# Kernel tuning notes

Hardware: AMD Instinct MI355X
Metric: run time of the kernel (lower is better)

Reference implementation:

```python
import jax, jax.numpy as jnp
import numpy as np

B, S, H, NH, DH, I, C, P = 4, 1024, 1280, 20, 64, 5120, 13, 8
LN_EPS = 1e-5


def setup_inputs() -> dict:
    key = jax.random.key(0)
    ks = jax.random.split(key, 20)
    n = lambda k, shp, s=0.02: (jax.random.normal(k, shp, jnp.float32) * s)
    return {
        "hidden_states": jax.random.normal(ks[0], (B, S, H), jnp.float32),
        "attention_mask": jnp.ones((B, S), jnp.float32),
        "Wq": n(ks[1], (H, H)), "bq": jnp.zeros((H,), jnp.float32),
        "Wk": n(ks[2], (H, H)), "bk": jnp.zeros((H,), jnp.float32),
        "Wv": n(ks[3], (H, H)), "bv": jnp.zeros((H,), jnp.float32),
        "W_ct1": n(ks[4], (P, C), 0.3), "b_ct1": jnp.zeros((P,), jnp.float32),
        "W_ct2": n(ks[5], (P, C), 0.3), "b_ct2": jnp.zeros((P,), jnp.float32),
        "M": n(ks[6], (C, C), 0.5),
        "bias_scale": jnp.full((1,), 0.5, jnp.float32),
        "W_ptm": n(ks[7], (P, H)), "b_ptm": jnp.zeros((P,), jnp.float32),
        "ln_g": jnp.ones((H,), jnp.float32), "ln_b": jnp.zeros((H,), jnp.float32),
        "Wf1": n(ks[8], (I, H)), "bf1": jnp.zeros((I,), jnp.float32),
        "Wf2": n(ks[9], (H, I)), "bf2": jnp.zeros((H,), jnp.float32),
    }


def reference(hidden_states, attention_mask, Wq, bq, Wk, bk, Wv, bv,
              W_ct1, b_ct1, W_ct2, b_ct2, M, bias_scale, W_ptm, b_ptm,
              ln_g, ln_b, Wf1, bf1, Wf2, bf2):
    h = hidden_states
    # crosstalk bilinear projection: (P,C) @ (C,P) -> (P,P)
    out1 = (M.T @ W_ct1.T + b_ct1).T          # (P, C)
    out2 = M @ W_ct2.T + b_ct2                # (C, P)
    R = out1 @ out2                           # (P, P)
    # ptm_predictor (Linear H->P) + softmax
    ptm = jax.nn.softmax(h @ W_ptm.T + b_ptm, axis=-1)            # (B,S,P)
    Bb = jnp.tanh(jnp.einsum('blc,cd,bmd->blm', ptm, R, ptm)) * bias_scale  # (B,S,S)
    # manual multi-head attention
    q = (h @ Wq.T + bq).reshape(B, S, NH, DH).transpose(0, 2, 1, 3)
    k = (h @ Wk.T + bk).reshape(B, S, NH, DH).transpose(0, 2, 1, 3)
    v = (h @ Wv.T + bv).reshape(B, S, NH, DH).transpose(0, 2, 1, 3)
    scores = jnp.einsum('bhld,bhmd->bhlm', q, k) / np.float32(np.sqrt(DH))
    scores = scores + Bb[:, None]
    scores = scores + (1.0 - attention_mask)[:, None, None, :] * jnp.finfo(h.dtype).min
    probs = jax.nn.softmax(scores, axis=-1)
    ctx = jnp.einsum('bhlm,bhmd->bhld', probs, v)
    ctx = ctx.transpose(0, 2, 1, 3).reshape(B, S, H)
    # residual + LayerNorm
    x = h + ctx
    mu = jnp.mean(x, -1, keepdims=True)
    var = jnp.var(x, -1, keepdims=True)
    x = (x - mu) * jax.lax.rsqrt(var + LN_EPS) * ln_g + ln_b
    # FFN with exact GELU, residual
    ff = jax.nn.gelu(x @ Wf1.T + bf1, approximate=False) @ Wf2.T + bf2
    return x + ff
```

## Files before the change

kernel.cpp:

```cpp
#include <hip/hip_runtime.h>
#include <math.h>

typedef _Float16 f16;
typedef _Float16 f16x2 __attribute__((ext_vector_type(2)));
typedef _Float16 f16x8 __attribute__((ext_vector_type(8)));
typedef _Float16 f16x4 __attribute__((ext_vector_type(4)));
typedef float f32x4 __attribute__((ext_vector_type(4)));

#define B_ 4
#define S_ 1024
#define H_ 1280
#define NH_ 20
#define DH_ 64
#define I_ 5120
#define C_ 13
#define P_ 8
#define QS_ 3840
#define LOG2E 1.44269504088896f

__device__ __forceinline__ void store_val(float* p, float v) { *p = v; }
__device__ __forceinline__ void store_val(f16* p, float v) { *p = (f16)v; }

__device__ __forceinline__ float fast_gelu(float x) {
    float ax = 0.70710678118654752f * fabsf(x);
    float t = __builtin_amdgcn_rcpf(1.0f + 0.3275911f * ax);
    float p = t * (0.254829592f + t * (-0.284496736f + t * (1.421413741f
              + t * (-1.453152027f + t * 1.061405429f))));
    float e = __builtin_exp2f(-(LOG2E) * ax * ax);
    float er = 1.0f - p * e;
    float cdf = 0.5f + 0.5f * (x >= 0.0f ? er : -er);
    return x * cdf;
}

__device__ __forceinline__ float fast_tanh(float x) {
    x = fminf(fmaxf(x, -20.0f), 20.0f);
    float e = __builtin_exp2f(x * (2.0f * LOG2E));
    return (e - 1.0f) * __builtin_amdgcn_rcpf(e + 1.0f);
}

__global__ __launch_bounds__(256) void cvt5_kernel(
    const float* __restrict__ s0, f16* __restrict__ d0, int n0,
    const float* __restrict__ s1, f16* __restrict__ d1, int n1,
    const float* __restrict__ s2, f16* __restrict__ d2, int n2,
    const float* __restrict__ s3, f16* __restrict__ d3, int n3,
    const float* __restrict__ s4, f16* __restrict__ d4, int n4) {
    int seg = blockIdx.y;
    const float* src = (seg == 0) ? s0 : (seg == 1) ? s1 : (seg == 2) ? s2
                     : (seg == 3) ? s3 : s4;
    f16* dst = (seg == 0) ? d0 : (seg == 1) ? d1 : (seg == 2) ? d2
             : (seg == 3) ? d3 : d4;
    int n = (seg == 0) ? n0 : (seg == 1) ? n1 : (seg == 2) ? n2
          : (seg == 3) ? n3 : n4;
    int i = blockIdx.x * 256 + threadIdx.x;
    if (i < n) {
        f32x4 v = ((const f32x4*)src)[i];
        f16x4 o;
#pragma unroll
        for (int e = 0; e < 4; e++) o[e] = (f16)v[e];
        ((f16x4*)dst)[i] = o;
    }
}

__global__ __launch_bounds__(256) void ptm_kernel(const float* __restrict__ hin,
                                                  const float* __restrict__ Wptm,
                                                  const float* __restrict__ bptm,
                                                  const float* __restrict__ Mg,
                                                  const float* __restrict__ W1,
                                                  const float* __restrict__ b1,
                                                  const float* __restrict__ W2,
                                                  const float* __restrict__ b2,
                                                  float* __restrict__ ptm,
                                                  float* __restrict__ tg,
                                                  f16* __restrict__ hin16) {
    __shared__ float o1[P_][C_];
    __shared__ float o2[C_][P_];
    __shared__ float R[P_ * P_];
    int t = threadIdx.x;
    if (t < P_ * C_) {
        int p = t / C_, c = t % C_;
        float s = b1[p];
        for (int k = 0; k < C_; k++) s += Mg[k * C_ + c] * W1[p * C_ + k];
        o1[p][c] = s;
        int c2 = t / P_, p2 = t % P_;
        float s2 = b2[p2];
        for (int k = 0; k < C_; k++) s2 += Mg[c2 * C_ + k] * W2[p2 * C_ + k];
        o2[c2][p2] = s2;
    }
    __syncthreads();
    if (t < P_ * P_) {
        int p = t >> 3, q = t & 7;
        float s = 0.f;
        for (int c = 0; c < C_; c++) s += o1[p][c] * o2[c][q];
        R[t] = s;
    }
    __syncthreads();

    int wv = t >> 6, lane = t & 63;
    int row = blockIdx.x * 4 + wv;
    const float* hrow = hin + (size_t)row * H_;
    f16* hrow16 = hin16 + (size_t)row * H_;
    float acc[P_] = {};
    for (int i = 0; i < H_ / 64; i++) {
        int k = lane + 64 * i;
        float hv = hrow[k];
        hrow16[k] = (f16)hv;
#pragma unroll
        for (int p = 0; p < P_; p++) acc[p] += hv * Wptm[p * H_ + k];
    }
#pragma unroll
    for (int p = 0; p < P_; p++) {
#pragma unroll
        for (int o = 32; o >= 1; o >>= 1) acc[p] += __shfl_xor(acc[p], o);
        acc[p] += bptm[p];
    }
    float mx = acc[0];
#pragma unroll
    for (int p = 1; p < P_; p++) mx = fmaxf(mx, acc[p]);
    float sum = 0.f;
#pragma unroll
    for (int p = 0; p < P_; p++) { acc[p] = expf(acc[p] - mx); sum += acc[p]; }
    float rinv = 1.f / sum;
#pragma unroll
    for (int p = 0; p < P_; p++) acc[p] *= rinv;
    float tv[P_];
#pragma unroll
    for (int d = 0; d < P_; d++) {
        float s = 0.f;
#pragma unroll
        for (int c = 0; c < P_; c++) s += acc[c] * R[c * P_ + d];
        tv[d] = s;
    }
    if (lane == 0) {
#pragma unroll
        for (int p = 0; p < P_; p++) {
            ptm[(size_t)row * P_ + p] = acc[p];
            tg[(size_t)row * P_ + p]  = tv[p];
        }
    }
}

__global__ __launch_bounds__(256) void bias_kernel(const float* __restrict__ tg,
                                                   const float* __restrict__ ptm,
                                                   const float* __restrict__ mask,
                                                   const float* __restrict__ bscale_p,
                                                   f16* __restrict__ bb) {
    const int bl = blockIdx.x;
    const int b = bl >> 10;
    const int t = threadIdx.x;
    __shared__ float tl[P_];
    if (t < P_) tl[t] = tg[(size_t)bl * P_ + t];
    __syncthreads();
    const float bscale = bscale_p[0];
    float t0 = tl[0], t1 = tl[1], t2 = tl[2], t3 = tl[3];
    float t4 = tl[4], t5 = tl[5], t6 = tl[6], t7 = tl[7];
#pragma unroll
    for (int i = 0; i < 4; i++) {
        int m = t + 256 * i;
        const float* pm = ptm + ((size_t)b * S_ + m) * P_;
        float4 p0 = *(const float4*)pm;
        float4 p1 = *(const float4*)(pm + 4);
        float d = t0 * p0.x + t1 * p0.y + t2 * p0.z + t3 * p0.w
                + t4 * p1.x + t5 * p1.y + t6 * p1.z + t7 * p1.w;
        float v = (fast_tanh(d) * bscale + (1.0f - mask[(size_t)b * S_ + m]) * (-30000.0f)) * LOG2E;
        bb[(size_t)bl * S_ + m] = (f16)v;
    }
}

template <int MODE, typename YT>
__device__ __forceinline__ void gemm_body(const f16* __restrict__ X,
                                          const f16* __restrict__ W,
                                          const float* __restrict__ bias,
                                          YT* __restrict__ Y,
                                          const f16* __restrict__ res,
                                          int Ndim, int Kdim, int kbeg, int kend,
                                          int m0, int n0, f16* sA, f16* sB) {
    const int t = threadIdx.x;
    const int lane = t & 63, w = t >> 6;
    const int wr = w >> 1, wc = w & 1;
    const int lr = lane & 15, kq = lane >> 4;

    f32x4 acc[4][4] = {};

    int s_row[4], s_gc[4];
#pragma unroll
    for (int inst = 0; inst < 4; inst++) {
        int ci = t + 256 * inst;
        s_row[inst] = ci >> 3;
        s_gc[inst] = (ci & 7) ^ (s_row[inst] & 7);
    }

    for (int k0 = kbeg; k0 < kend; k0 += 64) {
        __syncthreads();
#pragma unroll
        for (int inst = 0; inst < 4; inst++) {
            int ci = t + 256 * inst;
            __builtin_amdgcn_global_load_lds(
                (const unsigned*)(X + (size_t)(m0 + s_row[inst]) * Kdim + k0 + s_gc[inst] * 8),
                (unsigned*)(sA + ci * 8), 16, 0, 0);
        }
#pragma unroll
        for (int inst = 0; inst < 4; inst++) {
            int ci = t + 256 * inst;
            __builtin_amdgcn_global_load_lds(
                (const unsigned*)(W + (size_t)(n0 + s_row[inst]) * Kdim + k0 + s_gc[inst] * 8),
                (unsigned*)(sB + ci * 8), 16, 0, 0);
        }
        __syncthreads();
#pragma unroll
        for (int ks = 0; ks < 2; ks++) {
            f16x8 af[4], bf[4];
#pragma unroll
            for (int i = 0; i < 4; i++) {
                int row = wr * 64 + i * 16 + lr;
                int cl = (ks * 4 + kq) ^ (row & 7);
                af[i] = *(const f16x8*)(sA + row * 64 + cl * 8);
            }
#pragma unroll
            for (int j = 0; j < 4; j++) {
                int row = wc * 64 + j * 16 + lr;
                int cl = (ks * 4 + kq) ^ (row & 7);
                bf[j] = *(const f16x8*)(sB + row * 64 + cl * 8);
            }
#pragma unroll
            for (int i = 0; i < 4; i++)
#pragma unroll
                for (int j = 0; j < 4; j++)
                    acc[i][j] = __builtin_amdgcn_mfma_f32_16x16x32_f16(af[i], bf[j], acc[i][j], 0, 0, 0);
        }
    }
#pragma unroll
    for (int j = 0; j < 4; j++) {
        int col = n0 + wc * 64 + j * 16 + lr;
        float bcol = (MODE == 3) ? 0.f : bias[col];
#pragma unroll
        for (int i = 0; i < 4; i++) {
#pragma unroll
            for (int rr = 0; rr < 4; rr++) {
                int row = m0 + wr * 64 + i * 16 + kq * 4 + rr;
                float v = acc[i][j][rr] + bcol;
                if (MODE == 1) v = fast_gelu(v);
                store_val(&Y[(size_t)row * Ndim + col], v);
            }
        }
    }
}

template <int MODE, typename YT>
__global__ __launch_bounds__(256, 2) void gemm128(const f16* __restrict__ X,
                                                  const f16* __restrict__ W,
                                                  const float* __restrict__ bias,
                                                  YT* __restrict__ Y,
                                                  const f16* __restrict__ res,
                                                  int Ndim, int Kdim) {
    __shared__ f16 sA[128 * 64];
    __shared__ f16 sB[128 * 64];
    gemm_body<MODE, YT>(X, W, bias, Y, res, Ndim, Kdim, 0, Kdim,
                        blockIdx.x * 128, blockIdx.y * 128, sA, sB);
}

template <int MODE, typename YT>
__device__ __forceinline__ void g256_body(const f16* __restrict__ X,
                                          const f16* __restrict__ W,
                                          const float* __restrict__ bias,
                                          YT* __restrict__ Y,
                                          int Ndim, int Kdim, int kbeg, int kend,
                                          int m0, int n0, f16* sA, f16* sB) {
    const int NT = (kend - kbeg) >> 6;
    const int t = threadIdx.x;
    const int lane = t & 63, w = t >> 6;
    const int wr = w >> 2, wc = w & 3;
    const int lr = lane & 15, kq = lane >> 4;

    const int rh0 = t >> 3;
    const int gc0 = (t & 7) ^ (rh0 & 7);
    const f16* Asrc = X + (size_t)(m0 + rh0) * Kdim + kbeg + gc0 * 8;
    const f16* Bsrc = W + (size_t)(n0 + rh0) * Kdim + kbeg + gc0 * 8;

    f32x4 acc[8][4] = {};

#define STG_A(kt_) do { f16* d_ = sA + ((kt_) & 1) * 16384 + t * 8;            \
        const f16* s_ = Asrc + (size_t)(kt_) * 64;                             \
        __builtin_amdgcn_global_load_lds((const unsigned*)s_, (unsigned*)d_, 16, 0, 0); \
        __builtin_amdgcn_global_load_lds((const unsigned*)(s_ + (size_t)64 * Kdim),  (unsigned*)(d_ + 4096), 16, 0, 0);  \
        __builtin_amdgcn_global_load_lds((const unsigned*)(s_ + (size_t)128 * Kdim), (unsigned*)(d_ + 8192), 16, 0, 0);  \
        __builtin_amdgcn_global_load_lds((const unsigned*)(s_ + (size_t)192 * Kdim), (unsigned*)(d_ + 12288), 16, 0, 0); \
    } while (0)
#define STG_B(kt_) do { f16* d_ = sB + ((kt_) & 1) * 16384 + t * 8;            \
        const f16* s_ = Bsrc + (size_t)(kt_) * 64;                             \
        __builtin_amdgcn_global_load_lds((const unsigned*)s_, (unsigned*)d_, 16, 0, 0); \
        __builtin_amdgcn_global_load_lds((const unsigned*)(s_ + (size_t)64 * Kdim),  (unsigned*)(d_ + 4096), 16, 0, 0);  \
        __builtin_amdgcn_global_load_lds((const unsigned*)(s_ + (size_t)128 * Kdim), (unsigned*)(d_ + 8192), 16, 0, 0);  \
        __builtin_amdgcn_global_load_lds((const unsigned*)(s_ + (size_t)192 * Kdim), (unsigned*)(d_ + 12288), 16, 0, 0); \
    } while (0)

    STG_A(0); STG_B(0);
    if (NT > 1) {
        STG_A(1); STG_B(1);
        asm volatile("s_waitcnt vmcnt(8)");
    } else {
        asm volatile("s_waitcnt vmcnt(0)");
    }
    __builtin_amdgcn_s_barrier();

    for (int kt = 0; kt < NT; ++kt) {
        const int p = kt & 1;
        const f16* cA = sA + p * 16384;
        const f16* cB = sB + p * 16384;
        f16x8 a[4][2], b0[2][2], b1[2][2];

#pragma unroll
        for (int i = 0; i < 4; ++i) {
            const int r = wr * 128 + (i + 4) * 16 + lr;
#pragma unroll
            for (int ks = 0; ks < 2; ++ks)
                a[i][ks] = *(const f16x8*)(cA + r * 64 + (((ks * 4 + kq) ^ (r & 7)) * 8));
        }
#pragma unroll
        for (int j = 0; j < 2; ++j) {
            const int rb = wc * 64 + j * 16 + lr;
#pragma unroll
            for (int ks = 0; ks < 2; ++ks)
                b0[j][ks] = *(const f16x8*)(cB + rb * 64 + (((ks * 4 + kq) ^ (rb & 7)) * 8));
        }
        __builtin_amdgcn_s_barrier();
        __builtin_amdgcn_s_setprio(1);
#pragma unroll
        for (int ks = 0; ks < 2; ++ks)
#pragma unroll
            for (int i = 0; i < 4; ++i)
#pragma unroll
                for (int j = 0; j < 2; ++j)
                    acc[i + 4][j] = __builtin_amdgcn_mfma_f32_16x16x32_f16(
                        a[i][ks], b0[j][ks], acc[i + 4][j], 0, 0, 0);
        __builtin_amdgcn_s_setprio(0);
        __builtin_amdgcn_s_barrier();

#pragma unroll
        for (int j = 0; j < 2; ++j) {
            const int rb = wc * 64 + (j + 2) * 16 + lr;
#pragma unroll
            for (int ks = 0; ks < 2; ++ks)
                b1[j][ks] = *(const f16x8*)(cB + rb * 64 + (((ks * 4 + kq) ^ (rb & 7)) * 8));
        }
        __builtin_amdgcn_s_barrier();
        __builtin_amdgcn_s_setprio(1);
#pragma unroll
        for (int ks = 0; ks < 2; ++ks)
#pragma unroll
            for (int i = 0; i < 4; ++i)
#pragma unroll
                for (int j = 0; j < 2; ++j)
                    acc[i + 4][j + 2] = __builtin_amdgcn_mfma_f32_16x16x32_f16(
                        a[i][ks], b1[j][ks], acc[i + 4][j + 2], 0, 0, 0);
        __builtin_amdgcn_s_setprio(0);
        __builtin_amdgcn_s_barrier();

#pragma unroll
        for (int i = 0; i < 4; ++i) {
            const int r = wr * 128 + i * 16 + lr;
#pragma unroll
            for (int ks = 0; ks < 2; ++ks)
                a[i][ks] = *(const f16x8*)(cA + r * 64 + (((ks * 4 + kq) ^ (r & 7)) * 8));
        }
        if (kt + 2 < NT) STG_B(kt + 2);
        __builtin_amdgcn_s_barrier();
        __builtin_amdgcn_s_setprio(1);
#pragma unroll
        for (int ks = 0; ks < 2; ++ks)
#pragma unroll
            for (int i = 0; i < 4; ++i)
#pragma unroll
                for (int j = 0; j < 2; ++j)
                    acc[i][j] = __builtin_amdgcn_mfma_f32_16x16x32_f16(
                        a[i][ks], b0[j][ks], acc[i][j], 0, 0, 0);
        __builtin_amdgcn_s_setprio(0);
        __builtin_amdgcn_s_barrier();

        if (kt + 2 < NT) STG_A(kt + 2);
        __builtin_amdgcn_s_setprio(1);
#pragma unroll
        for (int ks = 0; ks < 2; ++ks)
#pragma unroll
            for (int i = 0; i < 4; ++i)
#pragma unroll
                for (int j = 0; j < 2; ++j)
                    acc[i][j + 2] = __builtin_amdgcn_mfma_f32_16x16x32_f16(
                        a[i][ks], b1[j][ks], acc[i][j + 2], 0, 0, 0);
        __builtin_amdgcn_s_setprio(0);
        if (kt + 2 < NT) asm volatile("s_waitcnt vmcnt(8)");
        else             asm volatile("s_waitcnt vmcnt(0)");
        __builtin_amdgcn_s_barrier();
    }
#undef STG_A
#undef STG_B

#pragma unroll
    for (int j = 0; j < 4; ++j) {
        const int col = n0 + wc * 64 + j * 16 + lr;
        const float bcol = (MODE == 3) ? 0.f : bias[col];
#pragma unroll
        for (int i = 0; i < 8; ++i) {
#pragma unroll
            for (int rr = 0; rr < 4; ++rr) {
                const int row = m0 + wr * 128 + i * 16 + kq * 4 + rr;
                float v = acc[i][j][rr] + bcol;
                store_val(&Y[(size_t)row * Ndim + col], v);
            }
        }
    }
}

__global__ __launch_bounds__(512, 2) void gemm256_sk(const f16* __restrict__ X,
                                                     const f16* __restrict__ W,
                                                     float* __restrict__ p0,
                                                     float* __restrict__ p1,
                                                     float* __restrict__ p2,
                                                     int Ndim, int Kdim) {
    __shared__ f16 sA[2 * 16384];
    __shared__ f16 sB[2 * 16384];
    const int z = blockIdx.z;
    float* __restrict__ Y = (z == 0) ? p0 : (z == 1) ? p1 : p2;
    const int kbeg = z * 1728;
    const int kend = (z == 2) ? Kdim : kbeg + 1728;
    g256_body<3, float>(X, W, nullptr, Y, Ndim, Kdim, kbeg, kend,
                        blockIdx.x * 256, blockIdx.y * 256, sA, sB);
}

__global__ __launch_bounds__(512, 2) void gemm256_qkv(const f16* __restrict__ X,
                                                      const f16* __restrict__ Wqkv,
                                                      const float* __restrict__ bq,
                                                      const float* __restrict__ bk,
                                                      const float* __restrict__ bv,
                                                      f16* __restrict__ Y) {
    __shared__ f16 sA[2 * 16384];
    __shared__ f16 sB[2 * 16384];
    const int nt = blockIdx.y;
    const int g = nt / 5;
    const float* bsel = (g == 0) ? bq : (g == 1) ? bk : bv;
    g256_body<0, f16>(X, Wqkv, bsel - (size_t)g * 1280, Y, QS_, H_, 0, H_,
                      blockIdx.x * 256, nt * 256, sA, sB);
}

__global__ __launch_bounds__(256) void reduce3_kernel(const float* __restrict__ p0,
                                                      const float* __restrict__ p1,
                                                      const float* __restrict__ p2,
                                                      const float* __restrict__ bias,
                                                      const f16* __restrict__ res,
                                                      float* __restrict__ out) {
    int i = blockIdx.x * 256 + threadIdx.x;
    int col = (i * 4) % H_;
    f32x4 a = ((const f32x4*)p0)[i];
    f32x4 b = ((const f32x4*)p1)[i];
    f32x4 c = ((const f32x4*)p2)[i];
    f32x4 bc = *(const f32x4*)(bias + col);
    f16x4 r = ((const f16x4*)res)[i];
    f32x4 o;
#pragma unroll
    for (int e = 0; e < 4; e++) o[e] = a[e] + b[e] + c[e] + bc[e] + (float)r[e];
    ((f32x4*)out)[i] = o;
}

__global__ __launch_bounds__(256) void attn_kernel(const f16* __restrict__ qkv,
                                                   const f16* __restrict__ bb,
                                                   const float* __restrict__ hin,
                                                   float* __restrict__ xpre) {
    __shared__ f16 sK[64 * 72];
    __shared__ f16 sVT[64 * 72];
    __shared__ f16 sP[64 * 72];

    const int t = threadIdx.x;
    const int w = t >> 6, lane = t & 63;
    const int lr = lane & 15, kq = lane >> 4;
    const int gid = blockIdx.x + 16 * (blockIdx.y + 20 * blockIdx.z);
    const int wk = (gid & 7) * 160 + (gid >> 3);
    const int l0 = (wk & 15) * 64;
    const int hb = wk >> 4;
    const int h = hb % 20, b = hb / 20;
    const size_t base  = (size_t)b * S_ * H_ + (size_t)h * DH_;
    const size_t baseq = (size_t)b * S_ * QS_ + (size_t)h * DH_;
    const size_t kbase = baseq + 1280;
    const size_t vbase = baseq + 2560;

    const int kr0 = t >> 3, kc8 = (t & 7) * 8;
    const int vr2 = (t >> 3) * 2, vc8 = (t & 7) * 8;
    const int vmsw = vr2 ^ vc8;
    const int br = t >> 2, bc16 = (t & 3) * 16;
    const f16* bbrow0 = bb + ((size_t)b * S_ + l0 + br) * S_;

    f16x8 kA0 = *(const f16x8*)&qkv[kbase + (size_t)kr0 * QS_ + kc8];
    f16x8 kA1 = *(const f16x8*)&qkv[kbase + (size_t)(kr0 + 32) * QS_ + kc8];
    f16x8 vA0 = *(const f16x8*)&qkv[vbase + (size_t)vr2 * QS_ + vc8];
    f16x8 vA1 = *(const f16x8*)&qkv[vbase + (size_t)(vr2 + 1) * QS_ + vc8];
    f16x8 bA0 = *(const f16x8*)(bbrow0 + bc16);
    f16x8 bA1 = *(const f16x8*)(bbrow0 + bc16 + 8);

    f16x8 afq[2];
#pragma unroll
    for (int ks = 0; ks < 2; ks++) {
        f16x8 qv = *(const f16x8*)&qkv[baseq + (size_t)(l0 + w * 16 + lr) * QS_ + ks * 32 + kq * 8];
#pragma unroll
        for (int e = 0; e < 8; e++) qv[e] = (f16)((float)qv[e] * (0.125f * LOG2E));
        afq[ks] = qv;
    }

    f32x4 acc_o[4] = {};
    float lstate[4] = {};

    for (int mt = 0; mt < 16; mt++) {
        __syncthreads();
        *(f16x8*)&sK[kr0 * 72 + kc8] = kA0;
        *(f16x8*)&sK[(kr0 + 32) * 72 + kc8] = kA1;
#pragma unroll
        for (int e = 0; e < 8; e++) {
            f16x2 pk = {vA0[e], vA1[e]};
            *(f16x2*)&sVT[(vc8 + e) * 72 + vmsw] = pk;
        }
        *(f16x8*)&sP[br * 72 + bc16] = bA0;
        *(f16x8*)&sP[br * 72 + bc16 + 8] = bA1;
        const int m1 = ((mt + 1) & 15) * 64;
        f16x8 kB0 = *(const f16x8*)&qkv[kbase + (size_t)(m1 + kr0) * QS_ + kc8];
        f16x8 kB1 = *(const f16x8*)&qkv[kbase + (size_t)(m1 + kr0 + 32) * QS_ + kc8];
        f16x8 vB0 = *(const f16x8*)&qkv[vbase + (size_t)(m1 + vr2) * QS_ + vc8];
        f16x8 vB1 = *(const f16x8*)&qkv[vbase + (size_t)(m1 + vr2 + 1) * QS_ + vc8];
        f16x8 bB0 = *(const f16x8*)(bbrow0 + m1 + bc16);
        f16x8 bB1 = *(const f16x8*)(bbrow0 + m1 + bc16 + 8);
        __syncthreads();

        f32x4 sacc[4] = {};
        __builtin_amdgcn_s_setprio(1);
#pragma unroll
        for (int ks = 0; ks < 2; ks++)
#pragma unroll
            for (int j = 0; j < 4; j++) {
                f16x8 bk = *(const f16x8*)&sK[(j * 16 + lr) * 72 + ks * 32 + kq * 8];
                sacc[j] = __builtin_amdgcn_mfma_f32_16x16x32_f16(afq[ks], bk, sacc[j], 0, 0, 0);
            }
        __builtin_amdgcn_s_setprio(0);

#pragma unroll
        for (int j = 0; j < 4; j++)
#pragma unroll
            for (int rr = 0; rr < 4; rr++) {
                const int sp_addr = (w * 16 + kq * 4 + rr) * 72 + j * 16 + lr;
                float p = __builtin_exp2f(sacc[j][rr] + (float)sP[sp_addr]);
                lstate[rr] += p;
                sP[sp_addr] = (f16)p;
            }

        f16x8 ap[2];
        ap[0] = *(const f16x8*)&sP[(w * 16 + lr) * 72 + kq * 8];
        ap[1] = *(const f16x8*)&sP[(w * 16 + lr) * 72 + 32 + kq * 8];
        __builtin_amdgcn_s_setprio(1);
#pragma unroll
        for (int ks = 0; ks < 2; ks++)
#pragma unroll
            for (int j2 = 0; j2 < 4; j2++) {
                int d = j2 * 16 + lr;
                int s_ = (d >> 3) & 7;
                f16x8 bv = *(const f16x8*)&sVT[d * 72 + 8 * (((ks << 2) + kq) ^ s_)];
                acc_o[j2] = __builtin_amdgcn_mfma_f32_16x16x32_f16(ap[ks], bv, acc_o[j2], 0, 0, 0);
            }
        __builtin_amdgcn_s_setprio(0);
        kA0 = kB0; kA1 = kB1; vA0 = vB0; vA1 = vB1; bA0 = bB0; bA1 = bB1;
    }

#pragma unroll
    for (int rr = 0; rr < 4; rr++) {
#pragma unroll
        for (int off = 8; off >= 1; off >>= 1) lstate[rr] += __shfl_xor(lstate[rr], off);
    }

#pragma unroll
    for (int rr = 0; rr < 4; rr++) {
        float linv = 1.0f / lstate[rr];
        int tok = l0 + w * 16 + kq * 4 + rr;
        size_t obase = base + (size_t)tok * H_;
#pragma unroll
        for (int j2 = 0; j2 < 4; j2++) {
            int d = j2 * 16 + lr;
            xpre[obase + d] = hin[obase + d] + acc_o[j2][rr] * linv;
        }
    }
}

__global__ __launch_bounds__(256) void ln_kernel(const float* __restrict__ xpre,
                                                 const float* __restrict__ g,
                                                 const float* __restrict__ bb,
                                                 f16* __restrict__ xln) {
    int row = blockIdx.x, t = threadIdx.x;
    const float* xr = xpre + (size_t)row * H_;
    float xv[5], s1 = 0.f, s2 = 0.f;
#pragma unroll
    for (int i = 0; i < 5; i++) {
        float v = xr[t + 256 * i];
        xv[i] = v; s1 += v; s2 += v * v;
    }
#pragma unroll
    for (int o = 32; o >= 1; o >>= 1) { s1 += __shfl_xor(s1, o); s2 += __shfl_xor(s2, o); }
    __shared__ float r1[4], r2[4];
    int wv = t >> 6, lane = t & 63;
    if (lane == 0) { r1[wv] = s1; r2[wv] = s2; }
    __syncthreads();
    float m1 = (r1[0] + r1[1] + r1[2] + r1[3]) * (1.0f / H_);
    float m2 = (r2[0] + r2[1] + r2[2] + r2[3]) * (1.0f / H_);
    float rstd = rsqrtf(m2 - m1 * m1 + 1e-5f);
#pragma unroll
    for (int i = 0; i < 5; i++) {
        int c = t + 256 * i;
        float v = (xv[i] - m1) * rstd * g[c] + bb[c];
        xln[(size_t)row * H_ + c] = (f16)v;
    }
}

extern "C" void kernel_launch(void* const* d_in, const int* in_sizes, int n_in,
                              void* d_out, int out_size, void* d_ws, size_t ws_size,
                              hipStream_t stream) {
    (void)in_sizes; (void)n_in; (void)out_size; (void)ws_size;
    const float* hin  = (const float*)d_in[0];
    const float* mask = (const float*)d_in[1];
    const float* Wq = (const float*)d_in[2];  const float* bq = (const float*)d_in[3];
    const float* Wk = (const float*)d_in[4];  const float* bk = (const float*)d_in[5];
    const float* Wv = (const float*)d_in[6];  const float* bv = (const float*)d_in[7];
    const float* Wct1 = (const float*)d_in[8];  const float* bct1 = (const float*)d_in[9];
    const float* Wct2 = (const float*)d_in[10]; const float* bct2 = (const float*)d_in[11];
    const float* Mg = (const float*)d_in[12];   const float* bscale = (const float*)d_in[13];
    const float* Wptm = (const float*)d_in[14]; const float* bptm = (const float*)d_in[15];
    const float* lng = (const float*)d_in[16];  const float* lnb = (const float*)d_in[17];
    const float* Wf1 = (const float*)d_in[18];  const float* bf1 = (const float*)d_in[19];
    const float* Wf2 = (const float*)d_in[20];  const float* bf2 = (const float*)d_in[21];

    char* ws = (char*)d_ws;
    const size_t SZ_PT  = (size_t)B_ * S_ * P_ * 4;
    const size_t SZ_H16 = (size_t)B_ * S_ * H_ * 2;
    const size_t SZ_H32 = (size_t)B_ * S_ * H_ * 4;
    const size_t SZ_WH  = (size_t)H_ * H_ * 2;
    const size_t SZ_WI  = (size_t)I_ * H_ * 2;
    float* ptm  = (float*)(ws + 256);
    float* tg   = (float*)(ws + 256 + SZ_PT);
    char* A0    = ws + 256 + 2 * SZ_PT;
    f16* hin16  = (f16*)(A0);
    f16* qkvb   = (f16*)(A0 + SZ_H16);
    float* xpre = (float*)(A0 + 4 * SZ_H16);
    f16* xln    = (f16*)(A0 + 4 * SZ_H16 + SZ_H32);
    f16* bbias  = (f16*)(A0 + 5 * SZ_H16 + SZ_H32);
    char* WA    = A0 + 5 * SZ_H16 + SZ_H32 + (size_t)B_ * S_ * S_ * 2;
    f16* Wq16   = (f16*)(WA);
    f16* Wk16   = (f16*)(WA + SZ_WH);
    f16* Wv16   = (f16*)(WA + 2 * SZ_WH);
    f16* Wf116  = (f16*)(WA + 3 * SZ_WH);
    f16* Wf216  = (f16*)(WA + 3 * SZ_WH + SZ_WI);
    f16* g1     = (f16*)(A0);
    float* pbuf = (float*)(WA + 3 * SZ_WH + 2 * SZ_WI);

    const int NW4 = (H_ * H_) / 4, NI4 = (I_ * H_) / 4;
    cvt5_kernel<<<dim3((NI4 + 255) / 256, 5), 256, 0, stream>>>(
        Wq, Wq16, NW4, Wk, Wk16, NW4, Wv, Wv16, NW4,
        Wf1, Wf116, NI4, Wf2, Wf216, NI4);

    ptm_kernel<<<S_ * B_ / 4, 256, 0, stream>>>(hin, Wptm, bptm,
                                                Mg, Wct1, bct1, Wct2, bct2, ptm, tg, hin16);
    bias_kernel<<<B_ * S_, 256, 0, stream>>>(tg, ptm, mask, bscale, bbias);
    gemm256_qkv<<<dim3(16, 15), 512, 0, stream>>>(hin16, Wq16, bq, bk, bv, qkvb);
    attn_kernel<<<dim3(S_ / 64, NH_, B_), 256, 0, stream>>>(qkvb, bbias, hin, xpre);
    ln_kernel<<<B_ * S_, 256, 0, stream>>>(xpre, lng, lnb, xln);
    gemm128<1, f16><<<dim3(32, I_ / 128), 256, 0, stream>>>(xln, Wf116, bf1, g1, nullptr, I_, H_);
    gemm256_sk<<<dim3(16, H_ / 256, 3), 512, 0, stream>>>(
        g1, Wf216, pbuf, pbuf + (size_t)B_ * S_ * H_, xpre, H_, I_);
    reduce3_kernel<<<(B_ * S_ * H_) / 4 / 256, 256, 0, stream>>>(
        pbuf, pbuf + (size_t)B_ * S_ * H_, xpre, bf2, xln, (float*)d_out);
}
```

Before: 455.5 us.

## Replace FFN1 GEMM with 256x320 pipelined tile kernel and merge prep kernels

```diff
diff --git a/kernel.cpp b/kernel.cpp
--- a/kernel.cpp
+++ b/kernel.cpp
@@ -38,44 +38,54 @@
     return (e - 1.0f) * __builtin_amdgcn_rcpf(e + 1.0f);
 }
 
-__global__ __launch_bounds__(256) void cvt5_kernel(
-    const float* __restrict__ s0, f16* __restrict__ d0, int n0,
-    const float* __restrict__ s1, f16* __restrict__ d1, int n1,
-    const float* __restrict__ s2, f16* __restrict__ d2, int n2,
-    const float* __restrict__ s3, f16* __restrict__ d3, int n3,
-    const float* __restrict__ s4, f16* __restrict__ d4, int n4) {
-    int seg = blockIdx.y;
-    const float* src = (seg == 0) ? s0 : (seg == 1) ? s1 : (seg == 2) ? s2
-                     : (seg == 3) ? s3 : s4;
-    f16* dst = (seg == 0) ? d0 : (seg == 1) ? d1 : (seg == 2) ? d2
-             : (seg == 3) ? d3 : d4;
-    int n = (seg == 0) ? n0 : (seg == 1) ? n1 : (seg == 2) ? n2
-          : (seg == 3) ? n3 : n4;
-    int i = blockIdx.x * 256 + threadIdx.x;
-    if (i < n) {
+__global__ __launch_bounds__(256) void prep_kernel(const float* __restrict__ hin,
+                                                   const float* __restrict__ Wptm,
+                                                   const float* __restrict__ bptm,
+                                                   const float* __restrict__ Mg,
+                                                   const float* __restrict__ W1,
+                                                   const float* __restrict__ b1,
+                                                   const float* __restrict__ W2,
+                                                   const float* __restrict__ b2,
+                                                   float* __restrict__ ptm,
+                                                   float* __restrict__ tg,
+                                                   f16* __restrict__ hin16,
+                                                   const float* __restrict__ Wq,
+                                                   const float* __restrict__ Wk,
+                                                   const float* __restrict__ Wv,
+                                                   const float* __restrict__ Wf1,
+                                                   const float* __restrict__ Wf2,
+                                                   f16* __restrict__ Wq16,
+                                                   f16* __restrict__ Wk16,
+                                                   f16* __restrict__ Wv16,
+                                                   f16* __restrict__ Wf116,
+                                                   f16* __restrict__ Wf216) {
+    const int bid = blockIdx.x;
+    int t = threadIdx.x;
+    if (bid >= 1024) {
+        const int cb = bid - 1024;
+        const float* src; f16* dst; int base;
+        if (cb < 4800) {
+            const int s = cb / 1600;
+            src = (s == 0) ? Wq : (s == 1) ? Wk : Wv;
+            dst = (s == 0) ? Wq16 : (s == 1) ? Wk16 : Wv16;
+            base = (cb - s * 1600) * 256;
+        } else if (cb < 11200) {
+            src = Wf1; dst = Wf116; base = (cb - 4800) * 256;
+        } else {
+            src = Wf2; dst = Wf216; base = (cb - 11200) * 256;
+        }
+        const int i = base + t;
         f32x4 v = ((const f32x4*)src)[i];
         f16x4 o;
 #pragma unroll
         for (int e = 0; e < 4; e++) o[e] = (f16)v[e];
         ((f16x4*)dst)[i] = o;
-    }
-}
-
-__global__ __launch_bounds__(256) void ptm_kernel(const float* __restrict__ hin,
-                                                  const float* __restrict__ Wptm,
-                                                  const float* __restrict__ bptm,
-                                                  const float* __restrict__ Mg,
-                                                  const float* __restrict__ W1,
-                                                  const float* __restrict__ b1,
-                                                  const float* __restrict__ W2,
-                                                  const float* __restrict__ b2,
-                                                  float* __restrict__ ptm,
-                                                  float* __restrict__ tg,
-                                                  f16* __restrict__ hin16) {
+        return;
+    }
+
     __shared__ float o1[P_][C_];
     __shared__ float o2[C_][P_];
     __shared__ float R[P_ * P_];
-    int t = threadIdx.x;
     if (t < P_ * C_) {
         int p = t / C_, c = t % C_;
         float s = b1[p];
@@ -96,7 +106,7 @@
     __syncthreads();
 
     int wv = t >> 6, lane = t & 63;
-    int row = blockIdx.x * 4 + wv;
+    int row = bid * 4 + wv;
     const float* hrow = hin + (size_t)row * H_;
     f16* hrow16 = hin16 + (size_t)row * H_;
     float acc[P_] = {};
@@ -167,98 +177,6 @@
 }
 
 template <int MODE, typename YT>
-__device__ __forceinline__ void gemm_body(const f16* __restrict__ X,
-                                          const f16* __restrict__ W,
-                                          const float* __restrict__ bias,
-                                          YT* __restrict__ Y,
-                                          const f16* __restrict__ res,
-                                          int Ndim, int Kdim, int kbeg, int kend,
-                                          int m0, int n0, f16* sA, f16* sB) {
-    const int t = threadIdx.x;
-    const int lane = t & 63, w = t >> 6;
-    const int wr = w >> 1, wc = w & 1;
-    const int lr = lane & 15, kq = lane >> 4;
-
-    f32x4 acc[4][4] = {};
-
-    int s_row[4], s_gc[4];
-#pragma unroll
-    for (int inst = 0; inst < 4; inst++) {
-        int ci = t + 256 * inst;
-        s_row[inst] = ci >> 3;
-        s_gc[inst] = (ci & 7) ^ (s_row[inst] & 7);
-    }
-
-    for (int k0 = kbeg; k0 < kend; k0 += 64) {
-        __syncthreads();
-#pragma unroll
-        for (int inst = 0; inst < 4; inst++) {
-            int ci = t + 256 * inst;
-            __builtin_amdgcn_global_load_lds(
-                (const unsigned*)(X + (size_t)(m0 + s_row[inst]) * Kdim + k0 + s_gc[inst] * 8),
-                (unsigned*)(sA + ci * 8), 16, 0, 0);
-        }
-#pragma unroll
-        for (int inst = 0; inst < 4; inst++) {
-            int ci = t + 256 * inst;
-            __builtin_amdgcn_global_load_lds(
-                (const unsigned*)(W + (size_t)(n0 + s_row[inst]) * Kdim + k0 + s_gc[inst] * 8),
-                (unsigned*)(sB + ci * 8), 16, 0, 0);
-        }
-        __syncthreads();
-#pragma unroll
-        for (int ks = 0; ks < 2; ks++) {
-            f16x8 af[4], bf[4];
-#pragma unroll
-            for (int i = 0; i < 4; i++) {
-                int row = wr * 64 + i * 16 + lr;
-                int cl = (ks * 4 + kq) ^ (row & 7);
-                af[i] = *(const f16x8*)(sA + row * 64 + cl * 8);
-            }
-#pragma unroll
-            for (int j = 0; j < 4; j++) {
-                int row = wc * 64 + j * 16 + lr;
-                int cl = (ks * 4 + kq) ^ (row & 7);
-                bf[j] = *(const f16x8*)(sB + row * 64 + cl * 8);
-            }
-#pragma unroll
-            for (int i = 0; i < 4; i++)
-#pragma unroll
-                for (int j = 0; j < 4; j++)
-                    acc[i][j] = __builtin_amdgcn_mfma_f32_16x16x32_f16(af[i], bf[j], acc[i][j], 0, 0, 0);
-        }
-    }
-#pragma unroll
-    for (int j = 0; j < 4; j++) {
-        int col = n0 + wc * 64 + j * 16 + lr;
-        float bcol = (MODE == 3) ? 0.f : bias[col];
-#pragma unroll
-        for (int i = 0; i < 4; i++) {
-#pragma unroll
-            for (int rr = 0; rr < 4; rr++) {
-                int row = m0 + wr * 64 + i * 16 + kq * 4 + rr;
-                float v = acc[i][j][rr] + bcol;
-                if (MODE == 1) v = fast_gelu(v);
-                store_val(&Y[(size_t)row * Ndim + col], v);
-            }
-        }
-    }
-}
-
-template <int MODE, typename YT>
-__global__ __launch_bounds__(256, 2) void gemm128(const f16* __restrict__ X,
-                                                  const f16* __restrict__ W,
-                                                  const float* __restrict__ bias,
-                                                  YT* __restrict__ Y,
-                                                  const f16* __restrict__ res,
-                                                  int Ndim, int Kdim) {
-    __shared__ f16 sA[128 * 64];
-    __shared__ f16 sB[128 * 64];
-    gemm_body<MODE, YT>(X, W, bias, Y, res, Ndim, Kdim, 0, Kdim,
-                        blockIdx.x * 128, blockIdx.y * 128, sA, sB);
-}
-
-template <int MODE, typename YT>
 __device__ __forceinline__ void g256_body(const f16* __restrict__ X,
                                           const f16* __restrict__ W,
                                           const float* __restrict__ bias,
@@ -439,6 +357,157 @@
     const float* bsel = (g == 0) ? bq : (g == 1) ? bk : bv;
     g256_body<0, f16>(X, Wqkv, bsel - (size_t)g * 1280, Y, QS_, H_, 0, H_,
                       blockIdx.x * 256, nt * 256, sA, sB);
+}
+
+__global__ __launch_bounds__(512, 2) void gemm256_f1(const f16* __restrict__ X,
+                                                     const f16* __restrict__ W,
+                                                     const float* __restrict__ bias,
+                                                     f16* __restrict__ Y) {
+    __shared__ f16 sA[2 * 16384];
+    __shared__ f16 sB[2 * 20480];
+    const int Kdim = H_;
+    const int NT = H_ / 64;
+    const int m0 = blockIdx.x * 256, n0 = blockIdx.y * 320;
+
+    const int t = threadIdx.x;
+    const int lane = t & 63, w = t >> 6;
+    const int wr = w >> 2, wc = w & 3;
+    const int lr = lane & 15, kq = lane >> 4;
+
+    const int rh0 = t >> 3;
+    const int gc0 = (t & 7) ^ (rh0 & 7);
+    const f16* Asrc = X + (size_t)(m0 + rh0) * Kdim + gc0 * 8;
+    const f16* Bsrc = W + (size_t)(n0 + rh0) * Kdim + gc0 * 8;
+
+    f32x4 acc[8][5] = {};
+
+#define F1_STG_A(kt_) do { f16* d_ = sA + ((kt_) & 1) * 16384 + t * 8;         \
+        const f16* s_ = Asrc + (size_t)(kt_) * 64;                             \
+        __builtin_amdgcn_global_load_lds((const unsigned*)s_, (unsigned*)d_, 16, 0, 0); \
+        __builtin_amdgcn_global_load_lds((const unsigned*)(s_ + (size_t)64 * Kdim),  (unsigned*)(d_ + 4096), 16, 0, 0);  \
+        __builtin_amdgcn_global_load_lds((const unsigned*)(s_ + (size_t)128 * Kdim), (unsigned*)(d_ + 8192), 16, 0, 0);  \
+        __builtin_amdgcn_global_load_lds((const unsigned*)(s_ + (size_t)192 * Kdim), (unsigned*)(d_ + 12288), 16, 0, 0); \
+    } while (0)
+#define F1_STG_B(kt_) do { f16* d_ = sB + ((kt_) & 1) * 20480 + t * 8;         \
+        const f16* s_ = Bsrc + (size_t)(kt_) * 64;                             \
+        __builtin_amdgcn_global_load_lds((const unsigned*)s_, (unsigned*)d_, 16, 0, 0); \
+        __builtin_amdgcn_global_load_lds((const unsigned*)(s_ + (size_t)64 * Kdim),  (unsigned*)(d_ + 4096), 16, 0, 0);  \
+        __builtin_amdgcn_global_load_lds((const unsigned*)(s_ + (size_t)128 * Kdim), (unsigned*)(d_ + 8192), 16, 0, 0);  \
+        __builtin_amdgcn_global_load_lds((const unsigned*)(s_ + (size_t)192 * Kdim), (unsigned*)(d_ + 12288), 16, 0, 0); \
+        __builtin_amdgcn_global_load_lds((const unsigned*)(s_ + (size_t)256 * Kdim), (unsigned*)(d_ + 16384), 16, 0, 0); \
+    } while (0)
+
+    F1_STG_A(0); F1_STG_B(0);
+    F1_STG_A(1); F1_STG_B(1);
+    asm volatile("s_waitcnt vmcnt(9)");
+    __builtin_amdgcn_s_barrier();
+
+    for (int kt = 0; kt < NT; ++kt) {
+        const int p = kt & 1;
+        const f16* cA = sA + p * 16384;
+        const f16* cB = sB + p * 20480;
+        f16x8 a[4][2], b0[3][2], b1[2][2];
+
+#pragma unroll
+        for (int i = 0; i < 4; ++i) {
+            const int r = wr * 128 + (i + 4) * 16 + lr;
+#pragma unroll
+            for (int ks = 0; ks < 2; ++ks)
+                a[i][ks] = *(const f16x8*)(cA + r * 64 + (((ks * 4 + kq) ^ (r & 7)) * 8));
+        }
+#pragma unroll
+        for (int j = 0; j < 3; ++j) {
+            const int rb = wc * 80 + j * 16 + lr;
+#pragma unroll
+            for (int ks = 0; ks < 2; ++ks)
+                b0[j][ks] = *(const f16x8*)(cB + rb * 64 + (((ks * 4 + kq) ^ (rb & 7)) * 8));
+        }
+        __builtin_amdgcn_s_barrier();
+        __builtin_amdgcn_s_setprio(1);
+#pragma unroll
+        for (int ks = 0; ks < 2; ++ks)
+#pragma unroll
+            for (int i = 0; i < 4; ++i)
+#pragma unroll
+                for (int j = 0; j < 3; ++j)
+                    acc[i + 4][j] = __builtin_amdgcn_mfma_f32_16x16x32_f16(
+                        a[i][ks], b0[j][ks], acc[i + 4][j], 0, 0, 0);
+        __builtin_amdgcn_s_setprio(0);
+        __builtin_amdgcn_s_barrier();
+
+#pragma unroll
+        for (int j = 0; j < 2; ++j) {
+            const int rb = wc * 80 + (j + 3) * 16 + lr;
+#pragma unroll
+            for (int ks = 0; ks < 2; ++ks)
+                b1[j][ks] = *(const f16x8*)(cB + rb * 64 + (((ks * 4 + kq) ^ (rb & 7)) * 8));
+        }
+        __builtin_amdgcn_s_barrier();
+        __builtin_amdgcn_s_setprio(1);
+#pragma unroll
+        for (int ks = 0; ks < 2; ++ks)
+#pragma unroll
+            for (int i = 0; i < 4; ++i)
+#pragma unroll
+                for (int j = 0; j < 2; ++j)
+                    acc[i + 4][j + 3] = __builtin_amdgcn_mfma_f32_16x16x32_f16(
+                        a[i][ks], b1[j][ks], acc[i + 4][j + 3], 0, 0, 0);
+        __builtin_amdgcn_s_setprio(0);
+        __builtin_amdgcn_s_barrier();
+
+#pragma unroll
+        for (int i = 0; i < 4; ++i) {
+            const int r = wr * 128 + i * 16 + lr;
+#pragma unroll
+            for (int ks = 0; ks < 2; ++ks)
+                a[i][ks] = *(const f16x8*)(cA + r * 64 + (((ks * 4 + kq) ^ (r & 7)) * 8));
+        }
+        if (kt + 2 < NT) F1_STG_B(kt + 2);
+        __builtin_amdgcn_s_barrier();
+        __builtin_amdgcn_s_setprio(1);
+#pragma unroll
+        for (int ks = 0; ks < 2; ++ks)
+#pragma unroll
+            for (int i = 0; i < 4; ++i)
+#pragma unroll
+                for (int j = 0; j < 3; ++j)
+                    acc[i][j] = __builtin_amdgcn_mfma_f32_16x16x32_f16(
+                        a[i][ks], b0[j][ks], acc[i][j], 0, 0, 0);
+        __builtin_amdgcn_s_setprio(0);
+        __builtin_amdgcn_s_barrier();
+
+        if (kt + 2 < NT) F1_STG_A(kt + 2);
+        __builtin_amdgcn_s_setprio(1);
+#pragma unroll
+        for (int ks = 0; ks < 2; ++ks)
+#pragma unroll
+            for (int i = 0; i < 4; ++i)
+#pragma unroll
+                for (int j = 0; j < 2; ++j)
+                    acc[i][j + 3] = __builtin_amdgcn_mfma_f32_16x16x32_f16(
+                        a[i][ks], b1[j][ks], acc[i][j + 3], 0, 0, 0);
+        __builtin_amdgcn_s_setprio(0);
+        if (kt + 2 < NT) asm volatile("s_waitcnt vmcnt(9)");
+        else             asm volatile("s_waitcnt vmcnt(0)");
+        __builtin_amdgcn_s_barrier();
+    }
+#undef F1_STG_A
+#undef F1_STG_B
+
+#pragma unroll
+    for (int j = 0; j < 5; ++j) {
+        const int col = n0 + wc * 80 + j * 16 + lr;
+        const float bcol = bias[col];
+#pragma unroll
+        for (int i = 0; i < 8; ++i) {
+#pragma unroll
+            for (int rr = 0; rr < 4; ++rr) {
+                const int row = m0 + wr * 128 + i * 16 + kq * 4 + rr;
+                float v = fast_gelu(acc[i][j][rr] + bcol);
+                Y[(size_t)row * I_ + col] = (f16)v;
+            }
+        }
+    }
 }
 
 __global__ __launch_bounds__(256) void reduce3_kernel(const float* __restrict__ p0,
@@ -652,18 +721,14 @@
     f16* g1     = (f16*)(A0);
     float* pbuf = (float*)(WA + 3 * SZ_WH + 2 * SZ_WI);
 
-    const int NW4 = (H_ * H_) / 4, NI4 = (I_ * H_) / 4;
-    cvt5_kernel<<<dim3((NI4 + 255) / 256, 5), 256, 0, stream>>>(
-        Wq, Wq16, NW4, Wk, Wk16, NW4, Wv, Wv16, NW4,
-        Wf1, Wf116, NI4, Wf2, Wf216, NI4);
-
-    ptm_kernel<<<S_ * B_ / 4, 256, 0, stream>>>(hin, Wptm, bptm,
-                                                Mg, Wct1, bct1, Wct2, bct2, ptm, tg, hin16);
+    prep_kernel<<<1024 + 17600, 256, 0, stream>>>(
+        hin, Wptm, bptm, Mg, Wct1, bct1, Wct2, bct2, ptm, tg, hin16,
+        Wq, Wk, Wv, Wf1, Wf2, Wq16, Wk16, Wv16, Wf116, Wf216);
     bias_kernel<<<B_ * S_, 256, 0, stream>>>(tg, ptm, mask, bscale, bbias);
     gemm256_qkv<<<dim3(16, 15), 512, 0, stream>>>(hin16, Wq16, bq, bk, bv, qkvb);
     attn_kernel<<<dim3(S_ / 64, NH_, B_), 256, 0, stream>>>(qkvb, bbias, hin, xpre);
     ln_kernel<<<B_ * S_, 256, 0, stream>>>(xpre, lng, lnb, xln);
-    gemm128<1, f16><<<dim3(32, I_ / 128), 256, 0, stream>>>(xln, Wf116, bf1, g1, nullptr, I_, H_);
+    gemm256_f1<<<dim3(16, 16), 512, 0, stream>>>(xln, Wf116, bf1, g1);
     gemm256_sk<<<dim3(16, H_ / 256, 3), 512, 0, stream>>>(
         g1, Wf216, pbuf, pbuf + (size_t)B_ * S_ * H_, xpre, H_, I_);
     reduce3_kernel<<<(B_ * S_ * H_) / 4 / 256, 256, 0, stream>>>(
```

Measured after the change: 427.7 us. -6.1%, faster.

## Fuse weight conversion into ptm kernel and store intermediates in fp16

Applied to the files above, without the earlier changes.

```diff
diff --git a/kernel.cpp b/kernel.cpp
--- a/kernel.cpp
+++ b/kernel.cpp
@@ -38,44 +38,54 @@
     return (e - 1.0f) * __builtin_amdgcn_rcpf(e + 1.0f);
 }
 
-__global__ __launch_bounds__(256) void cvt5_kernel(
-    const float* __restrict__ s0, f16* __restrict__ d0, int n0,
-    const float* __restrict__ s1, f16* __restrict__ d1, int n1,
-    const float* __restrict__ s2, f16* __restrict__ d2, int n2,
-    const float* __restrict__ s3, f16* __restrict__ d3, int n3,
-    const float* __restrict__ s4, f16* __restrict__ d4, int n4) {
-    int seg = blockIdx.y;
-    const float* src = (seg == 0) ? s0 : (seg == 1) ? s1 : (seg == 2) ? s2
-                     : (seg == 3) ? s3 : s4;
-    f16* dst = (seg == 0) ? d0 : (seg == 1) ? d1 : (seg == 2) ? d2
-             : (seg == 3) ? d3 : d4;
-    int n = (seg == 0) ? n0 : (seg == 1) ? n1 : (seg == 2) ? n2
-          : (seg == 3) ? n3 : n4;
-    int i = blockIdx.x * 256 + threadIdx.x;
-    if (i < n) {
+__global__ __launch_bounds__(256) void prep_kernel(const float* __restrict__ hin,
+                                                   const float* __restrict__ Wptm,
+                                                   const float* __restrict__ bptm,
+                                                   const float* __restrict__ Mg,
+                                                   const float* __restrict__ W1,
+                                                   const float* __restrict__ b1,
+                                                   const float* __restrict__ W2,
+                                                   const float* __restrict__ b2,
+                                                   float* __restrict__ ptm,
+                                                   float* __restrict__ tg,
+                                                   f16* __restrict__ hin16,
+                                                   const float* __restrict__ Wq,
+                                                   const float* __restrict__ Wk,
+                                                   const float* __restrict__ Wv,
+                                                   const float* __restrict__ Wf1,
+                                                   const float* __restrict__ Wf2,
+                                                   f16* __restrict__ Wq16,
+                                                   f16* __restrict__ Wk16,
+                                                   f16* __restrict__ Wv16,
+                                                   f16* __restrict__ Wf116,
+                                                   f16* __restrict__ Wf216) {
+    const int bid = blockIdx.x;
+    int t = threadIdx.x;
+    if (bid >= 1024) {
+        const int cb = bid - 1024;
+        const float* src; f16* dst; int base;
+        if (cb < 4800) {
+            const int s = cb / 1600;
+            src = (s == 0) ? Wq : (s == 1) ? Wk : Wv;
+            dst = (s == 0) ? Wq16 : (s == 1) ? Wk16 : Wv16;
+            base = (cb - s * 1600) * 256;
+        } else if (cb < 11200) {
+            src = Wf1; dst = Wf116; base = (cb - 4800) * 256;
+        } else {
+            src = Wf2; dst = Wf216; base = (cb - 11200) * 256;
+        }
+        const int i = base + t;
         f32x4 v = ((const f32x4*)src)[i];
         f16x4 o;
 #pragma unroll
         for (int e = 0; e < 4; e++) o[e] = (f16)v[e];
         ((f16x4*)dst)[i] = o;
-    }
-}
-
-__global__ __launch_bounds__(256) void ptm_kernel(const float* __restrict__ hin,
-                                                  const float* __restrict__ Wptm,
-                                                  const float* __restrict__ bptm,
-                                                  const float* __restrict__ Mg,
-                                                  const float* __restrict__ W1,
-                                                  const float* __restrict__ b1,
-                                                  const float* __restrict__ W2,
-                                                  const float* __restrict__ b2,
-                                                  float* __restrict__ ptm,
-                                                  float* __restrict__ tg,
-                                                  f16* __restrict__ hin16) {
+        return;
+    }
+
     __shared__ float o1[P_][C_];
     __shared__ float o2[C_][P_];
     __shared__ float R[P_ * P_];
-    int t = threadIdx.x;
     if (t < P_ * C_) {
         int p = t / C_, c = t % C_;
         float s = b1[p];
@@ -96,7 +106,7 @@
     __syncthreads();
 
     int wv = t >> 6, lane = t & 63;
-    int row = blockIdx.x * 4 + wv;
+    int row = bid * 4 + wv;
     const float* hrow = hin + (size_t)row * H_;
     f16* hrow16 = hin16 + (size_t)row * H_;
     float acc[P_] = {};
@@ -171,7 +181,6 @@
                                           const f16* __restrict__ W,
                                           const float* __restrict__ bias,
                                           YT* __restrict__ Y,
-                                          const f16* __restrict__ res,
                                           int Ndim, int Kdim, int kbeg, int kend,
                                           int m0, int n0, f16* sA, f16* sB) {
     const int t = threadIdx.x;
@@ -231,7 +240,7 @@
 #pragma unroll
     for (int j = 0; j < 4; j++) {
         int col = n0 + wc * 64 + j * 16 + lr;
-        float bcol = (MODE == 3) ? 0.f : bias[col];
+        float bcol = bias[col];
 #pragma unroll
         for (int i = 0; i < 4; i++) {
 #pragma unroll
@@ -250,11 +259,10 @@
                                                   const f16* __restrict__ W,
                                                   const float* __restrict__ bias,
                                                   YT* __restrict__ Y,
-                                                  const f16* __restrict__ res,
                                                   int Ndim, int Kdim) {
     __shared__ f16 sA[128 * 64];
     __shared__ f16 sB[128 * 64];
-    gemm_body<MODE, YT>(X, W, bias, Y, res, Ndim, Kdim, 0, Kdim,
+    gemm_body<MODE, YT>(X, W, bias, Y, Ndim, Kdim, 0, Kdim,
                         blockIdx.x * 128, blockIdx.y * 128, sA, sB);
 }
 
@@ -412,18 +420,18 @@
 
 __global__ __launch_bounds__(512, 2) void gemm256_sk(const f16* __restrict__ X,
                                                      const f16* __restrict__ W,
-                                                     float* __restrict__ p0,
-                                                     float* __restrict__ p1,
-                                                     float* __restrict__ p2,
+                                                     f16* __restrict__ p0,
+                                                     f16* __restrict__ p1,
+                                                     f16* __restrict__ p2,
                                                      int Ndim, int Kdim) {
     __shared__ f16 sA[2 * 16384];
     __shared__ f16 sB[2 * 16384];
     const int z = blockIdx.z;
-    float* __restrict__ Y = (z == 0) ? p0 : (z == 1) ? p1 : p2;
+    f16* __restrict__ Y = (z == 0) ? p0 : (z == 1) ? p1 : p2;
     const int kbeg = z * 1728;
     const int kend = (z == 2) ? Kdim : kbeg + 1728;
-    g256_body<3, float>(X, W, nullptr, Y, Ndim, Kdim, kbeg, kend,
-                        blockIdx.x * 256, blockIdx.y * 256, sA, sB);
+    g256_body<3, f16>(X, W, nullptr, Y, Ndim, Kdim, kbeg, kend,
+                      blockIdx.x * 256, blockIdx.y * 256, sA, sB);
 }
 
 __global__ __launch_bounds__(512, 2) void gemm256_qkv(const f16* __restrict__ X,
@@ -441,29 +449,30 @@
                       blockIdx.x * 256, nt * 256, sA, sB);
 }
 
-__global__ __launch_bounds__(256) void reduce3_kernel(const float* __restrict__ p0,
-                                                      const float* __restrict__ p1,
-                                                      const float* __restrict__ p2,
+__global__ __launch_bounds__(256) void reduce3_kernel(const f16* __restrict__ p0,
+                                                      const f16* __restrict__ p1,
+                                                      const f16* __restrict__ p2,
                                                       const float* __restrict__ bias,
                                                       const f16* __restrict__ res,
                                                       float* __restrict__ out) {
     int i = blockIdx.x * 256 + threadIdx.x;
     int col = (i * 4) % H_;
-    f32x4 a = ((const f32x4*)p0)[i];
-    f32x4 b = ((const f32x4*)p1)[i];
-    f32x4 c = ((const f32x4*)p2)[i];
+    f16x4 a = ((const f16x4*)p0)[i];
+    f16x4 b = ((const f16x4*)p1)[i];
+    f16x4 c = ((const f16x4*)p2)[i];
     f32x4 bc = *(const f32x4*)(bias + col);
     f16x4 r = ((const f16x4*)res)[i];
     f32x4 o;
 #pragma unroll
-    for (int e = 0; e < 4; e++) o[e] = a[e] + b[e] + c[e] + bc[e] + (float)r[e];
+    for (int e = 0; e < 4; e++)
+        o[e] = (float)a[e] + (float)b[e] + (float)c[e] + bc[e] + (float)r[e];
     ((f32x4*)out)[i] = o;
 }
 
 __global__ __launch_bounds__(256) void attn_kernel(const f16* __restrict__ qkv,
                                                    const f16* __restrict__ bb,
                                                    const float* __restrict__ hin,
-                                                   float* __restrict__ xpre) {
+                                                   f16* __restrict__ xpre) {
     __shared__ f16 sK[64 * 72];
     __shared__ f16 sVT[64 * 72];
     __shared__ f16 sP[64 * 72];
@@ -578,21 +587,21 @@
 #pragma unroll
         for (int j2 = 0; j2 < 4; j2++) {
             int d = j2 * 16 + lr;
-            xpre[obase + d] = hin[obase + d] + acc_o[j2][rr] * linv;
-        }
-    }
-}
-
-__global__ __launch_bounds__(256) void ln_kernel(const float* __restrict__ xpre,
+            xpre[obase + d] = (f16)(hin[obase + d] + acc_o[j2][rr] * linv);
+        }
+    }
+}
+
+__global__ __launch_bounds__(256) void ln_kernel(const f16* __restrict__ xpre,
                                                  const float* __restrict__ g,
                                                  const float* __restrict__ bb,
                                                  f16* __restrict__ xln) {
     int row = blockIdx.x, t = threadIdx.x;
-    const float* xr = xpre + (size_t)row * H_;
+    const f16* xr = xpre + (size_t)row * H_;
     float xv[5], s1 = 0.f, s2 = 0.f;
 #pragma unroll
     for (int i = 0; i < 5; i++) {
-        float v = xr[t + 256 * i];
+        float v = (float)xr[t + 256 * i];
         xv[i] = v; s1 += v; s2 += v * v;
     }
 #pragma unroll
@@ -640,7 +649,7 @@
     char* A0    = ws + 256 + 2 * SZ_PT;
     f16* hin16  = (f16*)(A0);
     f16* qkvb   = (f16*)(A0 + SZ_H16);
-    float* xpre = (float*)(A0 + 4 * SZ_H16);
+    f16* xpre   = (f16*)(A0 + 4 * SZ_H16);
     f16* xln    = (f16*)(A0 + 4 * SZ_H16 + SZ_H32);
     f16* bbias  = (f16*)(A0 + 5 * SZ_H16 + SZ_H32);
     char* WA    = A0 + 5 * SZ_H16 + SZ_H32 + (size_t)B_ * S_ * S_ * 2;
@@ -650,22 +659,20 @@
     f16* Wf116  = (f16*)(WA + 3 * SZ_WH);
     f16* Wf216  = (f16*)(WA + 3 * SZ_WH + SZ_WI);
     f16* g1     = (f16*)(A0);
-    float* pbuf = (float*)(WA + 3 * SZ_WH + 2 * SZ_WI);
-
-    const int NW4 = (H_ * H_) / 4, NI4 = (I_ * H_) / 4;
-    cvt5_kernel<<<dim3((NI4 + 255) / 256, 5), 256, 0, stream>>>(
-        Wq, Wq16, NW4, Wk, Wk16, NW4, Wv, Wv16, NW4,
-        Wf1, Wf116, NI4, Wf2, Wf216, NI4);
-
-    ptm_kernel<<<S_ * B_ / 4, 256, 0, stream>>>(hin, Wptm, bptm,
-                                                Mg, Wct1, bct1, Wct2, bct2, ptm, tg, hin16);
+    f16* pbuf   = (f16*)(WA + 3 * SZ_WH + 2 * SZ_WI);
+
+    prep_kernel<<<1024 + 17600, 256, 0, stream>>>(
+        hin, Wptm, bptm, Mg, Wct1, bct1, Wct2, bct2, ptm, tg, hin16,
+        Wq, Wk, Wv, Wf1, Wf2, Wq16, Wk16, Wv16, Wf116, Wf216);
     bias_kernel<<<B_ * S_, 256, 0, stream>>>(tg, ptm, mask, bscale, bbias);
     gemm256_qkv<<<dim3(16, 15), 512, 0, stream>>>(hin16, Wq16, bq, bk, bv, qkvb);
     attn_kernel<<<dim3(S_ / 64, NH_, B_), 256, 0, stream>>>(qkvb, bbias, hin, xpre);
     ln_kernel<<<B_ * S_, 256, 0, stream>>>(xpre, lng, lnb, xln);
-    gemm128<1, f16><<<dim3(32, I_ / 128), 256, 0, stream>>>(xln, Wf116, bf1, g1, nullptr, I_, H_);
+    gemm128<1, f16><<<dim3(32, I_ / 128), 256, 0, stream>>>(xln, Wf116, bf1, g1, I_, H_);
     gemm256_sk<<<dim3(16, H_ / 256, 3), 512, 0, stream>>>(
-        g1, Wf216, pbuf, pbuf + (size_t)B_ * S_ * H_, xpre, H_, I_);
+        g1, Wf216, pbuf, pbuf + (size_t)B_ * S_ * H_, pbuf + 2 * (size_t)B_ * S_ * H_,
+        H_, I_);
     reduce3_kernel<<<(B_ * S_ * H_) / 4 / 256, 256, 0, stream>>>(
-        pbuf, pbuf + (size_t)B_ * S_ * H_, xpre, bf2, xln, (float*)d_out);
-}
+        pbuf, pbuf + (size_t)B_ * S_ * H_, pbuf + 2 * (size_t)B_ * S_ * H_,
+        bf2, xln, (float*)d_out);
+}
```

Result: no change. 448.1 us (-1.6%).
